# Performance work log

Hardware: AMD Instinct MI355X
Metric: run time of the kernel (lower is better)

Reference implementation:

```python
import jax, jax.numpy as jnp
import numpy as np

EMB_DIM = 1024
N_HEADS = 16
HEAD_DIM = EMB_DIM // N_HEADS
WINDOW = 128
B, T = 4, 2048


def setup_inputs() -> dict:
    key = jax.random.key(0)
    k1, k2, k3 = jax.random.split(key, 3)
    x = jax.random.normal(k1, (B, T, EMB_DIM), dtype=jnp.float32)
    # nn.Linear weights: stored as [out, in], applied as x @ W^T
    s1 = 1.0 / np.sqrt(EMB_DIM)
    w_qkv = jax.random.uniform(k2, (3 * EMB_DIM, EMB_DIM), jnp.float32, -s1, s1)
    w_out = jax.random.uniform(k3, (EMB_DIM, EMB_DIM), jnp.float32, -s1, s1)
    return {"x": x, "w_qkv": w_qkv, "w_out": w_out}


def reference(x, w_qkv, w_out):
    Bs, Ts, C = x.shape
    scale = HEAD_DIM ** -0.5
    qkv = x @ w_qkv.T                                   # [B,T,3C]
    qkv = qkv.reshape(Bs, Ts, 3, N_HEADS, HEAD_DIM)
    qkv = jnp.transpose(qkv, (2, 0, 3, 1, 4))           # [3,B,H,T,D]
    q, k, v = qkv[0], qkv[1], qkv[2]
    scores = jnp.einsum('bhtd,bhsd->bhts', q, k) * scale  # [B,H,T,T]
    i = jnp.arange(Ts)[:, None]
    j = jnp.arange(Ts)[None, :]
    # causal AND within sliding window: i - WINDOW <= j <= i
    allowed = (j <= i) & (j >= i - WINDOW)               # [T,T] bool
    scores = jnp.where(allowed[None, None], scores, -jnp.inf)
    attn = jax.nn.softmax(scores, axis=-1)
    out = jnp.einsum('bhts,bhsd->bhtd', attn, v)         # [B,H,T,D]
    out = jnp.transpose(out, (0, 2, 1, 3)).reshape(Bs, Ts, C)
    return out @ w_out.T
```

## Files before the change

### kernel.cpp

```cpp
#include <hip/hip_runtime.h>
#include <hip/hip_bf16.h>
#include <stdint.h>

typedef __attribute__((ext_vector_type(8))) short bf16x8;
typedef __attribute__((ext_vector_type(4))) float f32x4;
typedef __attribute__((ext_vector_type(4))) unsigned short u16x4;

#define B_ 4
#define T_ 2048
#define C_ 1024
#define H_ 16
#define D_ 64

__device__ __forceinline__ unsigned short f2bf(float f) {
  union { float f; uint32_t u; } v; v.f = f;
  uint32_t u = v.u;
  uint32_t r = (u + 0x7FFFu + ((u >> 16) & 1u)) >> 16;
  return (unsigned short)r;
}

__global__ void __launch_bounds__(256) cast_f32_bf16(const float* __restrict__ src,
                                                     unsigned short* __restrict__ dst,
                                                     int n4) {
  int i = blockIdx.x * 256 + threadIdx.x;
  if (i >= n4) return;
  float4 f = ((const float4*)src)[i];
  u16x4 o;
  o[0] = f2bf(f.x); o[1] = f2bf(f.y); o[2] = f2bf(f.z); o[3] = f2bf(f.w);
  ((u16x4*)dst)[i] = o;
}

template <int MODE>
__global__ void __launch_bounds__(256) gemm_bt(const unsigned short* __restrict__ A,
                                               const unsigned short* __restrict__ Bm,
                                               unsigned short* __restrict__ qb,
                                               unsigned short* __restrict__ kb,
                                               unsigned short* __restrict__ vb,
                                               float* __restrict__ fo) {
  __shared__ short As[128 * 40];
  __shared__ short Bs[128 * 40];
  const int tid = threadIdx.x;
  const int bm = blockIdx.y * 128;
  const int bn = blockIdx.x * 128;
  const int wave = tid >> 6;
  const int l = tid & 63;
  const int wm = wave >> 1, wn = wave & 1;
  const int lm = l & 15, lq = l >> 4;
  const int r0 = tid >> 2;
  const int c0 = (tid & 3) << 3;

  f32x4 acc[4][4];
#pragma unroll
  for (int i = 0; i < 4; i++)
#pragma unroll
    for (int j = 0; j < 4; j++) acc[i][j] = (f32x4){0.f, 0.f, 0.f, 0.f};

  const unsigned short* Ap = A + (size_t)(bm + r0) * 1024 + c0;
  const unsigned short* Bp = Bm + (size_t)(bn + r0) * 1024 + c0;

  for (int k0 = 0; k0 < 1024; k0 += 32) {
    bf16x8 a0 = *(const bf16x8*)(Ap + k0);
    bf16x8 a1 = *(const bf16x8*)(Ap + (size_t)64 * 1024 + k0);
    bf16x8 b0 = *(const bf16x8*)(Bp + k0);
    bf16x8 b1 = *(const bf16x8*)(Bp + (size_t)64 * 1024 + k0);
    __syncthreads();
    *(bf16x8*)&As[r0 * 40 + c0] = a0;
    *(bf16x8*)&As[(r0 + 64) * 40 + c0] = a1;
    *(bf16x8*)&Bs[r0 * 40 + c0] = b0;
    *(bf16x8*)&Bs[(r0 + 64) * 40 + c0] = b1;
    __syncthreads();
    bf16x8 af[4], bfr[4];
#pragma unroll
    for (int i = 0; i < 4; i++)
      af[i] = *(const bf16x8*)&As[(wm * 64 + 16 * i + lm) * 40 + 8 * lq];
#pragma unroll
    for (int j = 0; j < 4; j++)
      bfr[j] = *(const bf16x8*)&Bs[(wn * 64 + 16 * j + lm) * 40 + 8 * lq];
#pragma unroll
    for (int i = 0; i < 4; i++)
#pragma unroll
      for (int j = 0; j < 4; j++)
        acc[i][j] = __builtin_amdgcn_mfma_f32_16x16x32_bf16(af[i], bfr[j], acc[i][j], 0, 0, 0);
  }

#pragma unroll
  for (int i = 0; i < 4; i++) {
#pragma unroll
    for (int j = 0; j < 4; j++) {
#pragma unroll
      for (int r = 0; r < 4; r++) {
        int m = bm + wm * 64 + 16 * i + 4 * lq + r;
        int n = bn + wn * 64 + 16 * j + lm;
        float val = acc[i][j][r];
        if (MODE == 0) {
          int which = n >> 10, rem = n & 1023;
          int h = rem >> 6, d = rem & 63;
          int b = m >> 11, t = m & 2047;
          unsigned short* dst = (which == 0) ? qb : ((which == 1) ? kb : vb);
          dst[(((size_t)(b * 16 + h)) * 2048 + t) * 64 + d] = f2bf(val);
        } else {
          fo[(size_t)m * 1024 + n] = val;
        }
      }
    }
  }
}

__global__ void __launch_bounds__(256) attn_swa(const unsigned short* __restrict__ Qb,
                                               const unsigned short* __restrict__ Kb,
                                               const unsigned short* __restrict__ Vb,
                                               unsigned short* __restrict__ Ob) {
  __shared__ short P[4][16 * 40];
  const int wv = threadIdx.x >> 6;
  const int l = threadIdx.x & 63;
  const int wid = blockIdx.x * 4 + wv;
  const int bh = wid >> 7;
  const int t0 = (wid & 127) << 4;
  const int lm = l & 15, lq = l >> 4;
  const size_t base = (size_t)bh * (T_ * D_);

  bf16x8 aq0 = *(const bf16x8*)(Qb + base + (size_t)(t0 + lm) * 64 + 8 * lq);
  bf16x8 aq1 = *(const bf16x8*)(Qb + base + (size_t)(t0 + lm) * 64 + 32 + 8 * lq);

  float mst[4], lst[4];
  f32x4 Oa[4];
#pragma unroll
  for (int r = 0; r < 4; r++) { mst[r] = -1e30f; lst[r] = 0.f; }
#pragma unroll
  for (int jt = 0; jt < 4; jt++) Oa[jt] = (f32x4){0.f, 0.f, 0.f, 0.f};

  const float cs = 0.125f * 1.44269504f;
  int jstart = t0 - 128; if (jstart < 0) jstart = 0;

  for (int j0 = jstart; j0 < t0 + 16; j0 += 32) {
    f32x4 S[2];
#pragma unroll
    for (int hh = 0; hh < 2; hh++) {
      int kr = j0 + 16 * hh + lm; if (kr > T_ - 1) kr = T_ - 1;
      bf16x8 bk0 = *(const bf16x8*)(Kb + base + (size_t)kr * 64 + 8 * lq);
      bf16x8 bk1 = *(const bf16x8*)(Kb + base + (size_t)kr * 64 + 32 + 8 * lq);
      f32x4 s = (f32x4){0.f, 0.f, 0.f, 0.f};
      s = __builtin_amdgcn_mfma_f32_16x16x32_bf16(aq0, bk0, s, 0, 0, 0);
      s = __builtin_amdgcn_mfma_f32_16x16x32_bf16(aq1, bk1, s, 0, 0, 0);
      S[hh] = s;
    }
    float p0s[4], p1s[4], al[4];
#pragma unroll
    for (int r = 0; r < 4; r++) {
      int t = t0 + 4 * lq + r;
      int ja = j0 + lm, jb = j0 + 16 + lm;
      float s0 = ((ja <= t) && (ja + 128 >= t)) ? S[0][r] * cs : -1e30f;
      float s1 = ((jb <= t) && (jb + 128 >= t)) ? S[1][r] * cs : -1e30f;
      float m2 = fmaxf(s0, s1);
#pragma unroll
      for (int off = 1; off < 16; off <<= 1) m2 = fmaxf(m2, __shfl_xor(m2, off));
      float mn = fmaxf(mst[r], m2);
      float a = __builtin_amdgcn_exp2f(mst[r] - mn);
      float p0 = __builtin_amdgcn_exp2f(s0 - mn);
      float p1 = __builtin_amdgcn_exp2f(s1 - mn);
      float ps = p0 + p1;
#pragma unroll
      for (int off = 1; off < 16; off <<= 1) ps += __shfl_xor(ps, off);
      lst[r] = lst[r] * a + ps;
      mst[r] = mn;
      al[r] = a; p0s[r] = p0; p1s[r] = p1;
    }
#pragma unroll
    for (int jt = 0; jt < 4; jt++)
#pragma unroll
      for (int r = 0; r < 4; r++) Oa[jt][r] *= al[r];
#pragma unroll
    for (int r = 0; r < 4; r++) {
      P[wv][(4 * lq + r) * 40 + lm] = (short)f2bf(p0s[r]);
      P[wv][(4 * lq + r) * 40 + 16 + lm] = (short)f2bf(p1s[r]);
    }
    bf16x8 pa = *(const bf16x8*)&P[wv][lm * 40 + 8 * lq];
#pragma unroll
    for (int jt = 0; jt < 4; jt++) {
      bf16x8 vf;
#pragma unroll
      for (int jj = 0; jj < 8; jj++) {
        int kk = j0 + 8 * lq + jj; if (kk > T_ - 1) kk = T_ - 1;
        vf[jj] = (short)Vb[base + (size_t)kk * 64 + 16 * jt + lm];
      }
      Oa[jt] = __builtin_amdgcn_mfma_f32_16x16x32_bf16(pa, vf, Oa[jt], 0, 0, 0);
    }
  }
  const int b = bh >> 4, h = bh & 15;
#pragma unroll
  for (int r = 0; r < 4; r++) {
    float inv = 1.0f / lst[r];
    int t = t0 + 4 * lq + r;
#pragma unroll
    for (int jt = 0; jt < 4; jt++) {
      int c = h * 64 + 16 * jt + lm;
      Ob[((size_t)(b * T_ + t)) * 1024 + c] = f2bf(Oa[jt][r] * inv);
    }
  }
}

extern "C" void kernel_launch(void* const* d_in, const int* in_sizes, int n_in,
                              void* d_out, int out_size, void* d_ws, size_t ws_size,
                              hipStream_t stream) {
  const float* x = (const float*)d_in[0];
  const float* w_qkv = (const float*)d_in[1];
  const float* w_out = (const float*)d_in[2];
  float* out = (float*)d_out;

  unsigned short* xb = (unsigned short*)d_ws;
  unsigned short* wqkvb = xb + (size_t)8192 * 1024;
  unsigned short* woutb = wqkvb + (size_t)3072 * 1024;
  unsigned short* qb = woutb + (size_t)1024 * 1024;
  unsigned short* kb = qb + (size_t)64 * 2048 * 64;
  unsigned short* vb = kb + (size_t)64 * 2048 * 64;

  cast_f32_bf16<<<8192, 256, 0, stream>>>(x, xb, 8192 * 1024 / 4);
  cast_f32_bf16<<<3072, 256, 0, stream>>>(w_qkv, wqkvb, 3072 * 1024 / 4);
  cast_f32_bf16<<<1024, 256, 0, stream>>>(w_out, woutb, 1024 * 1024 / 4);

  gemm_bt<0><<<dim3(24, 64), 256, 0, stream>>>(xb, wqkvb, qb, kb, vb, nullptr);

  attn_swa<<<2048, 256, 0, stream>>>(qb, kb, vb, xb);

  gemm_bt<1><<<dim3(8, 64), 256, 0, stream>>>(xb, woutb, nullptr, nullptr, nullptr, out);
}
```

Measured before the change: 232.7 us.

## Use direct global-to-LDS loads in GEMM and pre-transpose V for attention

The GEMM tile staging now uses global_load_lds to write straight into unpadded LDS instead of going through registers, removing the register round trip. A new transpose kernel lays V out as [bh, D, T], so the attention PV step reads one 16-byte vector per fragment instead of eight scalar 2-byte gathers. The costs are an extra kernel launch plus a full pass over V, and the unpadded 32-short LDS stride may raise bank conflicts on fragment reads. Workspace buffers are reused (V^T in xb, attention output in vb).

```diff
diff --git a/kernel.cpp b/kernel.cpp
--- a/kernel.cpp
+++ b/kernel.cpp
@@ -17,6 +17,11 @@
   uint32_t u = v.u;
   uint32_t r = (u + 0x7FFFu + ((u >> 16) & 1u)) >> 16;
   return (unsigned short)r;
+}
+
+__device__ __forceinline__ void gload_lds16(const unsigned short* g, short* l) {
+  __builtin_amdgcn_global_load_lds((__attribute__((address_space(1))) void*)(uintptr_t)g,
+                                   (__attribute__((address_space(3))) void*)l, 16, 0, 0);
 }
 
 __global__ void __launch_bounds__(256) cast_f32_bf16(const float* __restrict__ src,
@@ -37,17 +42,26 @@
                                                unsigned short* __restrict__ kb,
                                                unsigned short* __restrict__ vb,
                                                float* __restrict__ fo) {
-  __shared__ short As[128 * 40];
-  __shared__ short Bs[128 * 40];
+  __shared__ short As[128 * 32];
+  __shared__ short Bs[128 * 32];
   const int tid = threadIdx.x;
   const int bm = blockIdx.y * 128;
   const int bn = blockIdx.x * 128;
-  const int wave = tid >> 6;
+  const int w = tid >> 6;
   const int l = tid & 63;
-  const int wm = wave >> 1, wn = wave & 1;
+  const int wm = w >> 1, wn = w & 1;
   const int lm = l & 15, lq = l >> 4;
-  const int r0 = tid >> 2;
-  const int c0 = (tid & 3) << 3;
+
+  const int srow = w * 16 + (l >> 2);
+  const int scol = (l & 3) * 8;
+  const unsigned short* gA0 = A + (size_t)(bm + srow) * 1024 + scol;
+  const unsigned short* gA1 = gA0 + (size_t)64 * 1024;
+  const unsigned short* gB0 = Bm + (size_t)(bn + srow) * 1024 + scol;
+  const unsigned short* gB1 = gB0 + (size_t)64 * 1024;
+  short* dA0 = As + w * 512;
+  short* dA1 = As + 2048 + w * 512;
+  short* dB0 = Bs + w * 512;
+  short* dB1 = Bs + 2048 + w * 512;
 
   f32x4 acc[4][4];
 #pragma unroll
@@ -55,27 +69,20 @@
 #pragma unroll
     for (int j = 0; j < 4; j++) acc[i][j] = (f32x4){0.f, 0.f, 0.f, 0.f};
 
-  const unsigned short* Ap = A + (size_t)(bm + r0) * 1024 + c0;
-  const unsigned short* Bp = Bm + (size_t)(bn + r0) * 1024 + c0;
-
   for (int k0 = 0; k0 < 1024; k0 += 32) {
-    bf16x8 a0 = *(const bf16x8*)(Ap + k0);
-    bf16x8 a1 = *(const bf16x8*)(Ap + (size_t)64 * 1024 + k0);
-    bf16x8 b0 = *(const bf16x8*)(Bp + k0);
-    bf16x8 b1 = *(const bf16x8*)(Bp + (size_t)64 * 1024 + k0);
     __syncthreads();
-    *(bf16x8*)&As[r0 * 40 + c0] = a0;
-    *(bf16x8*)&As[(r0 + 64) * 40 + c0] = a1;
-    *(bf16x8*)&Bs[r0 * 40 + c0] = b0;
-    *(bf16x8*)&Bs[(r0 + 64) * 40 + c0] = b1;
+    gload_lds16(gA0 + k0, dA0);
+    gload_lds16(gA1 + k0, dA1);
+    gload_lds16(gB0 + k0, dB0);
+    gload_lds16(gB1 + k0, dB1);
     __syncthreads();
     bf16x8 af[4], bfr[4];
 #pragma unroll
     for (int i = 0; i < 4; i++)
-      af[i] = *(const bf16x8*)&As[(wm * 64 + 16 * i + lm) * 40 + 8 * lq];
+      af[i] = *(const bf16x8*)&As[(wm * 64 + 16 * i + lm) * 32 + 8 * lq];
 #pragma unroll
     for (int j = 0; j < 4; j++)
-      bfr[j] = *(const bf16x8*)&Bs[(wn * 64 + 16 * j + lm) * 40 + 8 * lq];
+      bfr[j] = *(const bf16x8*)&Bs[(wn * 64 + 16 * j + lm) * 32 + 8 * lq];
 #pragma unroll
     for (int i = 0; i < 4; i++)
 #pragma unroll
@@ -106,9 +113,37 @@
   }
 }
 
+__global__ void __launch_bounds__(256) transpose_v(const unsigned short* __restrict__ Vb,
+                                                   unsigned short* __restrict__ Vt) {
+  __shared__ unsigned short Ls[64 * 66];
+  const int tid = threadIdx.x;
+  const int bh = blockIdx.y;
+  const int t0 = blockIdx.x * 64;
+  const size_t base = (size_t)bh * (T_ * D_);
+  const int d0 = (tid & 7) * 8;
+  const int it = tid >> 3;
+#pragma unroll
+  for (int p = 0; p < 2; p++) {
+    int t = it + 32 * p;
+    bf16x8 v = *(const bf16x8*)(Vb + base + (size_t)(t0 + t) * 64 + d0);
+#pragma unroll
+    for (int e = 0; e < 8; e++) Ls[(d0 + e) * 66 + t] = (unsigned short)v[e];
+  }
+  __syncthreads();
+  const int d = tid >> 2;
+  const int c = tid & 3;
+  uint32_t r[8];
+  const uint32_t* Lw = (const uint32_t*)&Ls[d * 66 + c * 16];
+#pragma unroll
+  for (int wj = 0; wj < 8; wj++) r[wj] = Lw[wj];
+  unsigned short* o = Vt + base + (size_t)d * T_ + t0 + c * 16;
+  *(uint4*)o = *(const uint4*)&r[0];
+  *(uint4*)(o + 8) = *(const uint4*)&r[4];
+}
+
 __global__ void __launch_bounds__(256) attn_swa(const unsigned short* __restrict__ Qb,
                                                const unsigned short* __restrict__ Kb,
-                                               const unsigned short* __restrict__ Vb,
+                                               const unsigned short* __restrict__ Vt,
                                                unsigned short* __restrict__ Ob) {
   __shared__ short P[4][16 * 40];
   const int wv = threadIdx.x >> 6;
@@ -175,14 +210,11 @@
       P[wv][(4 * lq + r) * 40 + 16 + lm] = (short)f2bf(p1s[r]);
     }
     bf16x8 pa = *(const bf16x8*)&P[wv][lm * 40 + 8 * lq];
+    int tb = j0 + 8 * lq;
+    if (tb > T_ - 8) tb = T_ - 8;
 #pragma unroll
     for (int jt = 0; jt < 4; jt++) {
-      bf16x8 vf;
-#pragma unroll
-      for (int jj = 0; jj < 8; jj++) {
-        int kk = j0 + 8 * lq + jj; if (kk > T_ - 1) kk = T_ - 1;
-        vf[jj] = (short)Vb[base + (size_t)kk * 64 + 16 * jt + lm];
-      }
+      bf16x8 vf = *(const bf16x8*)(Vt + base + (size_t)(16 * jt + lm) * T_ + tb);
       Oa[jt] = __builtin_amdgcn_mfma_f32_16x16x32_bf16(pa, vf, Oa[jt], 0, 0, 0);
     }
   }
@@ -213,14 +245,15 @@
   unsigned short* qb = woutb + (size_t)1024 * 1024;
   unsigned short* kb = qb + (size_t)64 * 2048 * 64;
   unsigned short* vb = kb + (size_t)64 * 2048 * 64;
+  unsigned short* vtb = xb;
+  unsigned short* ob = vb;
 
   cast_f32_bf16<<<8192, 256, 0, stream>>>(x, xb, 8192 * 1024 / 4);
   cast_f32_bf16<<<3072, 256, 0, stream>>>(w_qkv, wqkvb, 3072 * 1024 / 4);
   cast_f32_bf16<<<1024, 256, 0, stream>>>(w_out, woutb, 1024 * 1024 / 4);
 
   gemm_bt<0><<<dim3(24, 64), 256, 0, stream>>>(xb, wqkvb, qb, kb, vb, nullptr);
-
-  attn_swa<<<2048, 256, 0, stream>>>(qb, kb, vb, xb);
-
-  gemm_bt<1><<<dim3(8, 64), 256, 0, stream>>>(xb, woutb, nullptr, nullptr, nullptr, out);
-}
+  transpose_v<<<dim3(32, 64), 256, 0, stream>>>(vb, vtb);
+  attn_swa<<<2048, 256, 0, stream>>>(qb, kb, vtb, ob);
+  gemm_bt<1><<<dim3(8, 64), 256, 0, stream>>>(ob, woutb, nullptr, nullptr, nullptr, out);
+}
```

Result: slower. 240.0 us (+3.1%).
